# Optimization experiments

Measured on AMD Instinct MI355X. Metric: run time of the kernel, lower is better.

## Reference

```python
import jax, jax.numpy as jnp
import numpy as np

S, D = 8192, 4096


def setup_inputs() -> dict:
    key = jax.random.key(0)
    k1, k2, k3 = jax.random.split(key, 3)
    inputs_embeds = jax.random.normal(k1, (S, D), dtype=jnp.float32)
    mask_1d = jax.random.randint(k2, (S,), 0, 2).astype(jnp.bool_)
    source = jax.random.normal(k3, (S, D), dtype=jnp.float32)
    return {"inputs_embeds": inputs_embeds, "mask_1d": mask_1d, "source": source}


def reference(inputs_embeds, mask_1d, source):
    # Old decomposition: broadcast mask over D, flatten to [S*D], cumsum on all
    # S*D elements (faithful to the original module's redundant full-length scan).
    mask_broad = jnp.broadcast_to(mask_1d[:, None], inputs_embeds.shape)  # [S, D]
    mask_flat = mask_broad.reshape(-1)            # [S*D] bool
    data_flat = inputs_embeds.reshape(-1)         # [S*D]
    source_flat = source.reshape(-1)              # [S*D]
    # S*D = 33.5M < 2^31, so int32 indices are safe.
    source_idx = jnp.cumsum(mask_flat.astype(jnp.int32)) - 1
    source_idx = jnp.clip(source_idx, 0, source_flat.shape[0] - 1)
    gathered = source_flat[source_idx]
    result_flat = jnp.where(mask_flat, gathered, data_flat)
    return result_flat.reshape(inputs_embeds.shape)
```

## Files before the change

### kernel.cpp

```cpp
#include <hip/hip_runtime.h>


typedef float f4 __attribute__((ext_vector_type(4)));

#define S_ROWS 8192
#define D4 1024
#define PREP_THREADS 256
#define ROWS_PER_THREAD (S_ROWS / PREP_THREADS)
#define GATHER_BLOCKS 2048
#define GATHER_THREADS 256
#define STRIDE (GATHER_BLOCKS * GATHER_THREADS)
#define TOTAL_F4 (S_ROWS * D4)
#define ITERS (TOTAL_F4 / STRIDE)

__global__ __launch_bounds__(PREP_THREADS) void prep_kernel(
    const void* __restrict__ mask_raw, const f4* __restrict__ in,
    const f4* __restrict__ src, const f4** __restrict__ rowptr) {
  __shared__ int s_not01, s_notF;
  __shared__ int sums[PREP_THREADS];
  __shared__ int excl[PREP_THREADS];
  const int t = threadIdx.x;
  if (t == 0) { s_not01 = 0; s_notF = 0; }
  __syncthreads();

  const unsigned int* w = (const unsigned int*)mask_raw;
  int not01 = 0, notF = 0;
  for (int i = t; i < S_ROWS / 4; i += PREP_THREADS) {
    const unsigned int v = w[i];
    not01 |= (v > 1u) ? 1 : 0;
    notF  |= (v != 0u && v != 0x3F800000u) ? 1 : 0;
  }
  if (not01) atomicOr(&s_not01, 1);
  if (notF)  atomicOr(&s_notF, 1);
  __syncthreads();
  const int mode = (!s_not01) ? 0 : ((!s_notF) ? 1 : 2);

  int vals[ROWS_PER_THREAD];
  const int base = t * ROWS_PER_THREAD;
  int local = 0;
  for (int k = 0; k < ROWS_PER_THREAD; ++k) {
    const int s = base + k;
    int mv;
    if (mode == 0)      mv = (((const int*)mask_raw)[s] != 0);
    else if (mode == 1) mv = (((const float*)mask_raw)[s] != 0.0f);
    else                mv = (((const unsigned char*)mask_raw)[s] != 0);
    vals[k] = mv;
    local += mv;
  }
  sums[t] = local;
  __syncthreads();
  if (t == 0) {
    int acc = 0;
    for (int i = 0; i < PREP_THREADS; ++i) { excl[i] = acc; acc += sums[i]; }
  }
  __syncthreads();
  int run = excl[t];
  for (int k = 0; k < ROWS_PER_THREAD; ++k) {
    const int s = base + k;
    rowptr[s] = vals[k] ? (src + (size_t)run * D4) : (in + (size_t)s * D4);
    run += vals[k];
  }
}

__global__ __launch_bounds__(GATHER_THREADS) void gather_kernel(
    const f4* const* __restrict__ rowptr, f4* __restrict__ out) {
  const int idx = blockIdx.x * GATHER_THREADS + threadIdx.x;
#pragma unroll
  for (int k = 0; k < ITERS; ++k) {
    const int i = idx + k * STRIDE;
    const f4* __restrict__ p = rowptr[i >> 10];
    const f4 v = p[i & 1023];
    __builtin_nontemporal_store(v, out + i);
  }
}

extern "C" void kernel_launch(void* const* d_in, const int* in_sizes, int n_in,
                              void* d_out, int out_size, void* d_ws, size_t ws_size,
                              hipStream_t stream) {
  const f4* inputs = (const f4*)d_in[0];
  const void* mask = d_in[1];
  const f4* source = (const f4*)d_in[2];
  f4* out = (f4*)d_out;
  const f4** rowptr = (const f4**)d_ws;

  prep_kernel<<<1, PREP_THREADS, 0, stream>>>(mask, inputs, source, rowptr);
  gather_kernel<<<GATHER_BLOCKS, GATHER_THREADS, 0, stream>>>(rowptr, out);
}
```

Baseline: 316.1 us.

## Assign two rows per block and load per-row source index once

The gather kernel now gives each block two whole rows, reads a per-row int source index once per block, and issues all loads before the stores. Previously every thread looked up a row pointer for each element with a grid-stride loop. This removes the repeated per-element pointer loads and packs more loads in flight per thread. It also drops the nontemporal stores in favour of ordinary stores, which may change cache behaviour, and launches many more blocks.

```diff
diff --git a/kernel.cpp b/kernel.cpp
--- a/kernel.cpp
+++ b/kernel.cpp
@@ -7,15 +7,13 @@
 #define D4 1024
 #define PREP_THREADS 256
 #define ROWS_PER_THREAD (S_ROWS / PREP_THREADS)
-#define GATHER_BLOCKS 2048
+#define ROWS_PER_BLOCK 2
+#define GATHER_BLOCKS (S_ROWS / ROWS_PER_BLOCK)
 #define GATHER_THREADS 256
-#define STRIDE (GATHER_BLOCKS * GATHER_THREADS)
-#define TOTAL_F4 (S_ROWS * D4)
-#define ITERS (TOTAL_F4 / STRIDE)
+#define F4_PER_THREAD (D4 / GATHER_THREADS)
 
 __global__ __launch_bounds__(PREP_THREADS) void prep_kernel(
-    const void* __restrict__ mask_raw, const f4* __restrict__ in,
-    const f4* __restrict__ src, const f4** __restrict__ rowptr) {
+    const void* __restrict__ mask_raw, int* __restrict__ rowsrc) {
   __shared__ int s_not01, s_notF;
   __shared__ int sums[PREP_THREADS];
   __shared__ int excl[PREP_THREADS];
@@ -57,21 +55,36 @@
   int run = excl[t];
   for (int k = 0; k < ROWS_PER_THREAD; ++k) {
     const int s = base + k;
-    rowptr[s] = vals[k] ? (src + (size_t)run * D4) : (in + (size_t)s * D4);
+    rowsrc[s] = vals[k] ? run : -1;
     run += vals[k];
   }
 }
 
 __global__ __launch_bounds__(GATHER_THREADS) void gather_kernel(
-    const f4* const* __restrict__ rowptr, f4* __restrict__ out) {
-  const int idx = blockIdx.x * GATHER_THREADS + threadIdx.x;
+    const f4* __restrict__ in, const f4* __restrict__ src,
+    const int* __restrict__ rowsrc, f4* __restrict__ out) {
+  const int s0 = blockIdx.x * ROWS_PER_BLOCK;
+  const int t = threadIdx.x;
+  const int r0 = rowsrc[s0];
+  const int r1 = rowsrc[s0 + 1];
+  const f4* __restrict__ p0 =
+      (r0 >= 0) ? (src + (size_t)r0 * D4) : (in + (size_t)s0 * D4);
+  const f4* __restrict__ p1 =
+      (r1 >= 0) ? (src + (size_t)r1 * D4) : (in + (size_t)(s0 + 1) * D4);
+  f4* __restrict__ o0 = out + (size_t)s0 * D4;
+  f4* __restrict__ o1 = o0 + D4;
+
+  f4 v[2 * F4_PER_THREAD];
 #pragma unroll
-  for (int k = 0; k < ITERS; ++k) {
-    const int i = idx + k * STRIDE;
-    const f4* __restrict__ p = rowptr[i >> 10];
-    const f4 v = p[i & 1023];
-    __builtin_nontemporal_store(v, out + i);
-  }
+  for (int k = 0; k < F4_PER_THREAD; ++k) v[k] = p0[t + k * GATHER_THREADS];
+#pragma unroll
+  for (int k = 0; k < F4_PER_THREAD; ++k)
+    v[F4_PER_THREAD + k] = p1[t + k * GATHER_THREADS];
+#pragma unroll
+  for (int k = 0; k < F4_PER_THREAD; ++k) o0[t + k * GATHER_THREADS] = v[k];
+#pragma unroll
+  for (int k = 0; k < F4_PER_THREAD; ++k)
+    o1[t + k * GATHER_THREADS] = v[F4_PER_THREAD + k];
 }
 
 extern "C" void kernel_launch(void* const* d_in, const int* in_sizes, int n_in,
@@ -81,8 +94,9 @@
   const void* mask = d_in[1];
   const f4* source = (const f4*)d_in[2];
   f4* out = (f4*)d_out;
-  const f4** rowptr = (const f4**)d_ws;
+  int* rowsrc = (int*)d_ws;
 
-  prep_kernel<<<1, PREP_THREADS, 0, stream>>>(mask, inputs, source, rowptr);
-  gather_kernel<<<GATHER_BLOCKS, GATHER_THREADS, 0, stream>>>(rowptr, out);
+  prep_kernel<<<1, PREP_THREADS, 0, stream>>>(mask, rowsrc);
+  gather_kernel<<<GATHER_BLOCKS, GATHER_THREADS, 0, stream>>>(
+      inputs, source, rowsrc, out);
 }
```

Result: faster. 298.9 us (-5.4%).
